# Kernel optimization log

Measured on AMD Instinct MI355X. Metric: run time of the kernel, lower is better.

## Reference

```python
import jax, jax.numpy as jnp
import numpy as np

B, S, HID, NH = 4, 2048, 2048, 16
HD = HID // NH
DECAY_INIT = 0.95


def setup_inputs() -> dict:
    key = jax.random.key(0)
    k1, k2, k3 = jax.random.split(key, 3)
    x = jax.random.normal(k1, (B, S, HID), jnp.float32)
    # torch Linear weights stored as [in, out] for x @ W; scaled like default init
    W_qkv = jax.random.normal(k2, (HID, 3 * HID), jnp.float32) / np.float32(np.sqrt(HID))
    W_out = jax.random.normal(k3, (HID, HID), jnp.float32) / np.float32(np.sqrt(HID))
    decay_param = jnp.full((NH,), DECAY_INIT, jnp.float32)
    kv0 = jnp.zeros((B, NH, HD), jnp.float32)
    k_sum0 = jnp.zeros((B, NH, HD), jnp.float32)
    attention_mask = jnp.ones((B, 1, 1, S), jnp.float32)
    return dict(x=x, kv0=kv0, k_sum0=k_sum0, attention_mask=attention_mask,
                W_qkv=W_qkv, W_out=W_out, decay_param=decay_param)


def _phi(u):
    # kernel feature map: elu(x) + 1 (non-negative)
    return jax.nn.elu(u) + 1.0


def reference(x, kv0, k_sum0, attention_mask, W_qkv, W_out, decay_param):
    b, s, hid = x.shape
    nh = decay_param.shape[0]
    hd = hid // nh
    qkv = x @ W_qkv                               # [b, s, 3*hid]
    q, k, v = jnp.split(qkv, 3, axis=-1)

    def to_time_major(t):                         # [b, s, hid] -> [s, b, nh, hd]
        return t.reshape(b, s, nh, hd).transpose(1, 0, 2, 3)

    q = _phi(to_time_major(q))
    k = _phi(to_time_major(k))
    v = to_time_major(v)

    # mask [b,1,1,s] -> [s, b, 1, 1]; padded tokens don't update the state
    m = attention_mask.reshape(b, 1, s, 1).transpose(2, 0, 1, 3)
    k = k * m
    v = v * m

    decay = jax.nn.sigmoid(decay_param)[None, :, None]  # [1, nh, 1]

    def step(carry, inp):
        kv, ks = carry                             # each [b, nh, hd]
        q_t, k_t, v_t = inp                        # each [b, nh, hd]
        kv = decay * kv + k_t * v_t
        ks = decay * ks + k_t
        num = jnp.sum(q_t * kv, axis=-1, keepdims=True)
        den = jnp.maximum(jnp.sum(q_t * ks, axis=-1, keepdims=True), 1e-6)
        return (kv, ks), (num / den) * q_t

    (kv, ks), outs = jax.lax.scan(step, (kv0, k_sum0), (q, k, v))
    out = outs.transpose(1, 0, 2, 3).reshape(b, s, hid) @ W_out
    return out, kv, ks
```

## Files before the change

kernel.cpp:

```cpp
#include <hip/hip_runtime.h>
#include <hip/hip_bf16.h>

typedef __hip_bfloat16 bf16;
typedef short bf16x8 __attribute__((ext_vector_type(8)));
typedef float f32x4 __attribute__((ext_vector_type(4)));

#define BB   4
#define SS   2048
#define HID  2048
#define NHD  16
#define HD   128
#define NCH  64
#define CHL  32

__device__ inline float sigm(float x) { return 1.f / (1.f + __expf(-x)); }
__device__ inline float phi_f(float v) { return v > 0.f ? v + 1.f : __expf(v); }

__device__ inline int probe_fp32(const void* probe) {
    return ((const unsigned*)probe)[0] != 0x3F733F73u;
}
__device__ inline float ldd(const void* p, int fp32, size_t i) {
    return fp32 ? ((const float*)p)[i] : __bfloat162float(((const bf16*)p)[i]);
}
__device__ inline void st_dual(void* p, int fp32, size_t i, float v) {
    if (fp32) ((float*)p)[i] = v;
    else      ((bf16*)p)[i] = __float2bfloat16(v);
}

__device__ inline void ld2(const bf16* p, float& a, float& b) {
    unsigned u = *(const unsigned*)p;
    union U { unsigned x; float f; } lo, hi;
    lo.x = u << 16; hi.x = u & 0xffff0000u;
    a = lo.f; b = hi.f;
}
__device__ inline void st2(bf16* p, float a, float b) {
    __hip_bfloat162 v;
    v.x = __float2bfloat16(a);
    v.y = __float2bfloat16(b);
    *(__hip_bfloat162*)p = v;
}

__device__ __forceinline__ void gload_lds16(const bf16* g, bf16* l) {
    __builtin_amdgcn_global_load_lds((const __attribute__((address_space(1))) void*)g,
                                     (__attribute__((address_space(3))) void*)l,
                                     16, 0, 0);
}

#define NB_CVT 16384
#define NB_T1  3072
#define NB_T2  1024
__global__ __launch_bounds__(256) void prep(const void* __restrict__ x,
                                            bf16* __restrict__ x_bf,
                                            const void* __restrict__ Wqkv,
                                            bf16* __restrict__ WqkvT,
                                            const void* __restrict__ Wout,
                                            bf16* __restrict__ WoutT,
                                            const void* __restrict__ probe) {
    int fp32 = probe_fp32(probe);
    int bid = blockIdx.x;
    int tid = threadIdx.x;
    if (bid < NB_CVT) {
        size_t i = ((size_t)bid * 256 + tid) * 4;
        if (fp32) {
            float4 v = *(const float4*)((const float*)x + i);
            bf16* o = x_bf + i;
            o[0] = __float2bfloat16(v.x); o[1] = __float2bfloat16(v.y);
            o[2] = __float2bfloat16(v.z); o[3] = __float2bfloat16(v.w);
        } else {
            *(short4*)(x_bf + i) = *(const short4*)((const bf16*)x + i);
        }
        return;
    }
    const void* in; bf16* out; int R, C, idx;
    if (bid < NB_CVT + NB_T1) {
        in = Wqkv; out = WqkvT; R = HID; C = 3 * HID; idx = bid - NB_CVT;
    } else {
        in = Wout; out = WoutT; R = HID; C = HID; idx = bid - NB_CVT - NB_T1;
    }
    int ctiles = C / 64;
    int c0 = (idx % ctiles) * 64;
    int r0 = (idx / ctiles) * 64;
    __shared__ bf16 t[64][65];
    int c = tid & 63;
    int rb = tid >> 6;
#pragma unroll
    for (int i = 0; i < 16; i++) {
        int r = rb + i * 4;
        t[r][c] = __float2bfloat16(ldd(in, fp32, (size_t)(r0 + r) * C + c0 + c));
    }
    __syncthreads();
#pragma unroll
    for (int i = 0; i < 16; i++) {
        int r = rb + i * 4;
        out[(size_t)(c0 + r) * R + r0 + c] = t[c][r];
    }
}

template <int MH>
__device__ __forceinline__ void lda_frags(const short* ldsA, bf16x8 (&af)[4][2],
                                          int wm2, int l15, int quad, int sw) {
#pragma unroll
    for (int i = 0; i < 4; i++) {
#pragma unroll
        for (int s = 0; s < 2; s++)
            af[i][s] = *(const bf16x8*)&ldsA[(MH * 128 + wm2 + i * 16 + l15) * 64 +
                                             (((quad + 4 * s) ^ sw) << 3)];
    }
}
template <int NH>
__device__ __forceinline__ void ldb_frags(const short* ldsB, bf16x8 (&bfr)[2][2],
                                          int wn2, int l15, int quad, int sw) {
#pragma unroll
    for (int j = 0; j < 2; j++) {
#pragma unroll
        for (int s = 0; s < 2; s++)
            bfr[j][s] = *(const bf16x8*)&ldsB[(NH * 128 + wn2 + j * 16 + l15) * 64 +
                                              (((quad + 4 * s) ^ sw) << 3)];
    }
}
template <int MH, int NH>
__device__ __forceinline__ void mma_quad(f32x4 (&acc)[2][2][4][2],
                                         const bf16x8 (&af)[4][2],
                                         const bf16x8 (&bfr)[2][2]) {
    __builtin_amdgcn_s_setprio(1);
#pragma unroll
    for (int s = 0; s < 2; s++)
#pragma unroll
        for (int i = 0; i < 4; i++)
#pragma unroll
            for (int j = 0; j < 2; j++)
                acc[MH][NH][i][j] = __builtin_amdgcn_mfma_f32_16x16x32_bf16(
                    af[i][s], bfr[j][s], acc[MH][NH][i][j], 0, 0, 0);
    __builtin_amdgcn_s_setprio(0);
}

template <int EPI>
__global__ __launch_bounds__(512) void gemm256(const bf16* __restrict__ A,
                                               const bf16* __restrict__ Bt,
                                               void* __restrict__ Cv,
                                               const void* __restrict__ mask,
                                               const void* __restrict__ probe,
                                               int M, int N, int K) {
    int fp32 = probe_fp32(probe);
    __shared__ __align__(16) short lds[2][2][256 * 64];
    const int tid = threadIdx.x;
    const int lane = tid & 63, wave = tid >> 6;
    const int quad = lane >> 4, l15 = lane & 15;
    const int sw = l15 & 7;
    const int wm2 = ((wave >> 2) & 1) * 64;
    const int wn2 = (wave & 3) * 32;
    const int m0 = blockIdx.y * 256, n0 = blockIdx.x * 256;
    const int KT = K >> 6;

    const int rl = lane >> 3, pu = lane & 7;
    const bf16* gAb = A  + (size_t)(m0 + wave * 8 + rl) * K + ((pu ^ rl) << 3);
    const bf16* gBb = Bt + (size_t)(n0 + wave * 8 + rl) * K + ((pu ^ rl) << 3);

    auto stageA = [&](int bufi, int h, int kt) {
        if (kt >= KT) return;
        const bf16* g = gAb + (size_t)(h * 128) * K + kt * 64;
        gload_lds16(g,                  (bf16*)&lds[bufi][0][(h * 128 + wave * 8) * 64]);
        gload_lds16(g + (size_t)64 * K, (bf16*)&lds[bufi][0][(h * 128 + 64 + wave * 8) * 64]);
    };
    auto stageB = [&](int bufi, int h, int kt) {
        if (kt >= KT) return;
        const bf16* g = gBb + (size_t)(h * 128) * K + kt * 64;
        gload_lds16(g,                  (bf16*)&lds[bufi][1][(h * 128 + wave * 8) * 64]);
        gload_lds16(g + (size_t)64 * K, (bf16*)&lds[bufi][1][(h * 128 + 64 + wave * 8) * 64]);
    };

    f32x4 acc[2][2][4][2];
    f32x4 zero = {0.f, 0.f, 0.f, 0.f};
#pragma unroll
    for (int a = 0; a < 2; a++)
#pragma unroll
        for (int b = 0; b < 2; b++)
#pragma unroll
            for (int i = 0; i < 4; i++)
#pragma unroll
                for (int j = 0; j < 2; j++) acc[a][b][i][j] = zero;
    bf16x8 af[4][2], bfr[2][2];

    stageA(0, 0, 0); stageB(0, 1, 0); stageA(0, 1, 0); stageB(0, 0, 0);
    stageA(1, 0, 1); stageB(1, 1, 1);
    asm volatile("s_waitcnt vmcnt(4)" ::: "memory");
    __builtin_amdgcn_s_barrier();

#define PH_SYNC_MFMA(MH, NH)                                                   \
    __builtin_amdgcn_sched_barrier(0);                                         \
    __builtin_amdgcn_s_barrier();                                              \
    asm volatile("s_waitcnt lgkmcnt(0)" ::: "memory");                         \
    __builtin_amdgcn_sched_barrier(0);                                         \
    mma_quad<MH, NH>(acc, af, bfr);                                            \
    __builtin_amdgcn_s_barrier();

#define TILE_BODY(BUF, kt)                                                     \
    {                                                                          \
        const short* ldsA = &lds[BUF][0][0];                                   \
        const short* ldsB = &lds[BUF][1][0];                                   \
                    \
        lda_frags<0>(ldsA, af, wm2, l15, quad, sw);                            \
        ldb_frags<0>(ldsB, bfr, wn2, l15, quad, sw);                           \
        stageA((BUF) ^ 1, 1, (kt) + 1);                                        \
        asm volatile("s_waitcnt lgkmcnt(8)" ::: "memory");                     \
        PH_SYNC_MFMA(0, 0)                                                     \
                            \
        ldb_frags<1>(ldsB, bfr, wn2, l15, quad, sw);                           \
        stageB((BUF) ^ 1, 0, (kt) + 1);                                        \
        PH_SYNC_MFMA(0, 1)                                                     \
           \
        lda_frags<1>(ldsA, af, wm2, l15, quad, sw);                            \
        stageA((BUF), 0, (kt) + 2);                                            \
        PH_SYNC_MFMA(1, 1)                                                     \
                         \
        ldb_frags<0>(ldsB, bfr, wn2, l15, quad, sw);                           \
        stageB((BUF), 1, (kt) + 2);                                            \
        __builtin_amdgcn_sched_barrier(0);                                     \
        __builtin_amdgcn_s_barrier();                                          \
        asm volatile("s_waitcnt lgkmcnt(0)" ::: "memory");                     \
        __builtin_amdgcn_sched_barrier(0);                                     \
        mma_quad<1, 0>(acc, af, bfr);                                          \
             \
        if ((kt) + 2 < KT) { asm volatile("s_waitcnt vmcnt(4)" ::: "memory"); }\
        else               { asm volatile("s_waitcnt vmcnt(0)" ::: "memory"); }\
        __builtin_amdgcn_s_barrier();                                          \
    }

    for (int kt = 0; kt < KT; kt += 2) {
        TILE_BODY(0, kt)
        TILE_BODY(1, kt + 1)
    }
#undef TILE_BODY
#undef PH_SYNC_MFMA

#pragma unroll
    for (int mh = 0; mh < 2; mh++)
#pragma unroll
        for (int i = 0; i < 4; i++)
#pragma unroll
            for (int r = 0; r < 4; r++) {
                int m = m0 + mh * 128 + wm2 + i * 16 + quad * 4 + r;
                float mk = 1.f;
                if (EPI) mk = ldd(mask, fp32, m);
#pragma unroll
                for (int nh = 0; nh < 2; nh++)
#pragma unroll
                    for (int j = 0; j < 2; j++) {
                        int n = n0 + nh * 128 + wn2 + j * 16 + l15;
                        float v = acc[mh][nh][i][j][r];
                        if (EPI) {
                            if (n < HID)          v = phi_f(v);
                            else if (n < 2 * HID) v = phi_f(v) * mk;
                            else                  v = v * mk;
                            ((bf16*)Cv)[(size_t)m * N + n] = __float2bfloat16(v);
                        } else {
                            st_dual(Cv, fp32, (size_t)m * N + n, v);
                        }
                    }
            }
}

__global__ __launch_bounds__(64) void scan_local(const bf16* __restrict__ qkv,
                                                 float* __restrict__ ckv,
                                                 float* __restrict__ cks,
                                                 const void* __restrict__ decp) {
    int fp32 = probe_fp32(decp);
    int blk = blockIdx.x;
    int bh = blk / NCH, c = blk % NCH;
    int b = bh >> 4, h = bh & 15;
    int lane = threadIdx.x;
    int hd = lane * 2;
    float dec = sigm(ldd(decp, fp32, h));
    const bf16* kb = qkv + (size_t)(b * SS + c * CHL) * (3 * HID) + HID + h * HD + hd;
    const bf16* vb = kb + HID;
    float kv0 = 0.f, kv1 = 0.f, ks0 = 0.f, ks1 = 0.f;
    for (int t = 0; t < CHL; t++) {
        float k0, k1, v0, v1;
        ld2(kb, k0, k1);
        ld2(vb, v0, v1);
        kb += 3 * HID; vb += 3 * HID;
        kv0 = dec * kv0 + k0 * v0;
        kv1 = dec * kv1 + k1 * v1;
        ks0 = dec * ks0 + k0;
        ks1 = dec * ks1 + k1;
    }
    int o = blk * HD + hd;
    ckv[o] = kv0; ckv[o + 1] = kv1;
    cks[o] = ks0; cks[o + 1] = ks1;
}

__global__ __launch_bounds__(64) void scan_out(const bf16* __restrict__ qkv,
                                               const float* __restrict__ ckv,
                                               const float* __restrict__ cks,
                                               const void* __restrict__ kv0in,
                                               const void* __restrict__ ks0in,
                                               const void* __restrict__ decp,
                                               bf16* __restrict__ outs,
                                               void* __restrict__ outbase) {
    int fp32 = probe_fp32(decp);
    int blk = blockIdx.x;
    int bh = blk / NCH, c = blk % NCH;
    int b = bh >> 4, h = bh & 15;
    int lane = threadIdx.x;
    int hd = lane * 2;
    float dec = sigm(ldd(decp, fp32, h));
    float dl = powf(dec, (float)CHL);

    float kva = ldd(kv0in, fp32, bh * HD + hd);
    float kvb = ldd(kv0in, fp32, bh * HD + hd + 1);
    float ksa = ldd(ks0in, fp32, bh * HD + hd);
    float ksb = ldd(ks0in, fp32, bh * HD + hd + 1);
    for (int j = 0; j < c; j++) {
        int o = (bh * NCH + j) * HD + hd;
        kva = dl * kva + ckv[o];
        kvb = dl * kvb + ckv[o + 1];
        ksa = dl * ksa + cks[o];
        ksb = dl * ksb + cks[o + 1];
    }

    const bf16* qb = qkv + (size_t)(b * SS + c * CHL) * (3 * HID) + h * HD + hd;
    const bf16* kb = qb + HID;
    const bf16* vb = qb + 2 * HID;
    bf16* ob = outs + (size_t)(b * SS + c * CHL) * HID + h * HD + hd;
    for (int t = 0; t < CHL; t++) {
        float q0, q1, k0, k1, v0, v1;
        ld2(qb, q0, q1);
        ld2(kb, k0, k1);
        ld2(vb, v0, v1);
        qb += 3 * HID; kb += 3 * HID; vb += 3 * HID;
        kva = dec * kva + k0 * v0;
        kvb = dec * kvb + k1 * v1;
        ksa = dec * ksa + k0;
        ksb = dec * ksb + k1;
        float num = q0 * kva + q1 * kvb;
        float den = q0 * ksa + q1 * ksb;
#pragma unroll
        for (int off = 32; off > 0; off >>= 1) {
            num += __shfl_xor(num, off);
            den += __shfl_xor(den, off);
        }
        float sc = num / fmaxf(den, 1e-6f);
        st2(ob, q0 * sc, q1 * sc);
        ob += HID;
    }

    if (c == NCH - 1) {
        size_t base = (size_t)BB * SS * HID;
        st_dual(outbase, fp32, base + bh * HD + hd, kva);
        st_dual(outbase, fp32, base + bh * HD + hd + 1, kvb);
        st_dual(outbase, fp32, base + BB * NHD * HD + bh * HD + hd, ksa);
        st_dual(outbase, fp32, base + BB * NHD * HD + bh * HD + hd + 1, ksb);
    }
}

extern "C" void kernel_launch(void* const* d_in, const int* in_sizes, int n_in,
                              void* d_out, int out_size, void* d_ws, size_t ws_size,
                              hipStream_t stream) {
    const void* x    = d_in[0];
    const void* kv0  = d_in[1];
    const void* ks0  = d_in[2];
    const void* am   = d_in[3];
    const void* Wqkv = d_in[4];
    const void* Wout = d_in[5];
    const void* decp = d_in[6];

    const int M = BB * SS;
    const int N1 = 3 * HID;
    const int K = HID;

    char* ws = (char*)d_ws;
    bf16* WqkvT = (bf16*)ws;  ws += (size_t)N1 * K * 2;
    bf16* WoutT = (bf16*)ws;  ws += (size_t)HID * HID * 2;
    bf16* x_bf  = (bf16*)ws;  ws += (size_t)M * HID * 2;
    bf16* qkvb  = (bf16*)ws;  ws += (size_t)M * N1 * 2;
    bf16* outs  = (bf16*)ws;  ws += (size_t)M * HID * 2;
    float* ckv  = (float*)ws; ws += (size_t)BB * NHD * NCH * HD * 4;
    float* cks  = (float*)ws; ws += (size_t)BB * NHD * NCH * HD * 4;

    prep<<<NB_CVT + NB_T1 + NB_T2, 256, 0, stream>>>(x, x_bf, Wqkv, WqkvT,
                                                     Wout, WoutT, decp);

    gemm256<1><<<dim3(N1 / 256, M / 256), 512, 0, stream>>>(x_bf, WqkvT, qkvb, am, decp,
                                                            M, N1, K);

    scan_local<<<BB * NHD * NCH, 64, 0, stream>>>(qkvb, ckv, cks, decp);
    scan_out<<<BB * NHD * NCH, 64, 0, stream>>>(qkvb, ckv, cks, kv0, ks0, decp,
                                                outs, d_out);

    gemm256<0><<<dim3(HID / 256, M / 256), 512, 0, stream>>>(outs, WoutT, d_out, nullptr,
                                                             decp, M, HID, K);
}
```

Before: 505.1 us.

## Halve scan chunk length and pack two chunks per wavefront with 4-wide loads

The chunked linear-attention scan now uses 128 chunks of 16 steps instead of 64 chunks of 32, which halves the serial per-chunk recurrence. Each 64-lane wavefront now handles two (batch,head,chunk) items, with each lane covering 4 head dims through 8-byte bf16 loads and stores and float4 chunk-state accesses. The shuffle reduction shrinks to 5 steps. The cost is a longer serial prefix over preceding chunk states in scan_out (up to 127 iterations) and twice as many chunk-state reads.

```diff
diff --git a/kernel.cpp b/kernel.cpp
--- a/kernel.cpp
+++ b/kernel.cpp
@@ -10,8 +10,8 @@
 #define HID  2048
 #define NHD  16
 #define HD   128
-#define NCH  64
-#define CHL  32
+#define NCH  128
+#define CHL  16
 
 __device__ inline float sigm(float x) { return 1.f / (1.f + __expf(-x)); }
 __device__ inline float phi_f(float v) { return v > 0.f ? v + 1.f : __expf(v); }
@@ -27,17 +27,21 @@
     else      ((bf16*)p)[i] = __float2bfloat16(v);
 }
 
-__device__ inline void ld2(const bf16* p, float& a, float& b) {
-    unsigned u = *(const unsigned*)p;
-    union U { unsigned x; float f; } lo, hi;
-    lo.x = u << 16; hi.x = u & 0xffff0000u;
-    a = lo.f; b = hi.f;
-}
-__device__ inline void st2(bf16* p, float a, float b) {
-    __hip_bfloat162 v;
-    v.x = __float2bfloat16(a);
-    v.y = __float2bfloat16(b);
-    *(__hip_bfloat162*)p = v;
+__device__ inline void ld4b(const bf16* p, float& a, float& b, float& c, float& d) {
+    uint2 u = *(const uint2*)p;
+    union U { unsigned x; float f; } t;
+    t.x = u.x << 16;          a = t.f;
+    t.x = u.x & 0xffff0000u;  b = t.f;
+    t.x = u.y << 16;          c = t.f;
+    t.x = u.y & 0xffff0000u;  d = t.f;
+}
+__device__ inline void st4b(bf16* p, float a, float b, float c, float d) {
+    __hip_bfloat162 lo, hi;
+    lo.x = __float2bfloat16(a); lo.y = __float2bfloat16(b);
+    hi.x = __float2bfloat16(c); hi.y = __float2bfloat16(d);
+    uint2 u;
+    u.x = *(unsigned*)&lo; u.y = *(unsigned*)&hi;
+    *(uint2*)p = u;
 }
 
 __device__ __forceinline__ void gload_lds16(const bf16* g, bf16* l) {
@@ -265,28 +269,30 @@
                                                  float* __restrict__ cks,
                                                  const void* __restrict__ decp) {
     int fp32 = probe_fp32(decp);
-    int blk = blockIdx.x;
-    int bh = blk / NCH, c = blk % NCH;
+    int lane = threadIdx.x;
+    int p = blockIdx.x * 2 + (lane >> 5);
+    int c = p >> 6;
+    int bh = p & 63;
     int b = bh >> 4, h = bh & 15;
-    int lane = threadIdx.x;
-    int hd = lane * 2;
+    int hd = (lane & 31) * 4;
     float dec = sigm(ldd(decp, fp32, h));
     const bf16* kb = qkv + (size_t)(b * SS + c * CHL) * (3 * HID) + HID + h * HD + hd;
     const bf16* vb = kb + HID;
-    float kv0 = 0.f, kv1 = 0.f, ks0 = 0.f, ks1 = 0.f;
+    float kv0 = 0.f, kv1 = 0.f, kv2 = 0.f, kv3 = 0.f;
+    float ks0 = 0.f, ks1 = 0.f, ks2 = 0.f, ks3 = 0.f;
     for (int t = 0; t < CHL; t++) {
-        float k0, k1, v0, v1;
-        ld2(kb, k0, k1);
-        ld2(vb, v0, v1);
+        float k0, k1, k2, k3, v0, v1, v2, v3;
+        ld4b(kb, k0, k1, k2, k3);
+        ld4b(vb, v0, v1, v2, v3);
         kb += 3 * HID; vb += 3 * HID;
-        kv0 = dec * kv0 + k0 * v0;
-        kv1 = dec * kv1 + k1 * v1;
-        ks0 = dec * ks0 + k0;
-        ks1 = dec * ks1 + k1;
-    }
-    int o = blk * HD + hd;
-    ckv[o] = kv0; ckv[o + 1] = kv1;
-    cks[o] = ks0; cks[o + 1] = ks1;
+        kv0 = dec * kv0 + k0 * v0;  kv1 = dec * kv1 + k1 * v1;
+        kv2 = dec * kv2 + k2 * v2;  kv3 = dec * kv3 + k3 * v3;
+        ks0 = dec * ks0 + k0;       ks1 = dec * ks1 + k1;
+        ks2 = dec * ks2 + k2;       ks3 = dec * ks3 + k3;
+    }
+    size_t o = (size_t)(bh * NCH + c) * HD + hd;
+    *(float4*)&ckv[o] = make_float4(kv0, kv1, kv2, kv3);
+    *(float4*)&cks[o] = make_float4(ks0, ks1, ks2, ks3);
 }
 
 __global__ __launch_bounds__(64) void scan_out(const bf16* __restrict__ qkv,
@@ -298,24 +304,31 @@
                                                bf16* __restrict__ outs,
                                                void* __restrict__ outbase) {
     int fp32 = probe_fp32(decp);
-    int blk = blockIdx.x;
-    int bh = blk / NCH, c = blk % NCH;
+    int lane = threadIdx.x;
+    int p = blockIdx.x * 2 + (lane >> 5);
+    int c = p >> 6;
+    int bh = p & 63;
     int b = bh >> 4, h = bh & 15;
-    int lane = threadIdx.x;
-    int hd = lane * 2;
+    int hd = (lane & 31) * 4;
     float dec = sigm(ldd(decp, fp32, h));
     float dl = powf(dec, (float)CHL);
 
     float kva = ldd(kv0in, fp32, bh * HD + hd);
     float kvb = ldd(kv0in, fp32, bh * HD + hd + 1);
+    float kvc = ldd(kv0in, fp32, bh * HD + hd + 2);
+    float kvd = ldd(kv0in, fp32, bh * HD + hd + 3);
     float ksa = ldd(ks0in, fp32, bh * HD + hd);
     float ksb = ldd(ks0in, fp32, bh * HD + hd + 1);
+    float ksc = ldd(ks0in, fp32, bh * HD + hd + 2);
+    float ksd = ldd(ks0in, fp32, bh * HD + hd + 3);
     for (int j = 0; j < c; j++) {
-        int o = (bh * NCH + j) * HD + hd;
-        kva = dl * kva + ckv[o];
-        kvb = dl * kvb + ckv[o + 1];
-        ksa = dl * ksa + cks[o];
-        ksb = dl * ksb + cks[o + 1];
+        size_t o = (size_t)(bh * NCH + j) * HD + hd;
+        float4 fv = *(const float4*)&ckv[o];
+        float4 fs = *(const float4*)&cks[o];
+        kva = dl * kva + fv.x;  kvb = dl * kvb + fv.y;
+        kvc = dl * kvc + fv.z;  kvd = dl * kvd + fv.w;
+        ksa = dl * ksa + fs.x;  ksb = dl * ksb + fs.y;
+        ksc = dl * ksc + fs.z;  ksd = dl * ksd + fs.w;
     }
 
     const bf16* qb = qkv + (size_t)(b * SS + c * CHL) * (3 * HID) + h * HD + hd;
@@ -323,33 +336,37 @@
     const bf16* vb = qb + 2 * HID;
     bf16* ob = outs + (size_t)(b * SS + c * CHL) * HID + h * HD + hd;
     for (int t = 0; t < CHL; t++) {
-        float q0, q1, k0, k1, v0, v1;
-        ld2(qb, q0, q1);
-        ld2(kb, k0, k1);
-        ld2(vb, v0, v1);
+        float q0, q1, q2, q3, k0, k1, k2, k3, v0, v1, v2, v3;
+        ld4b(qb, q0, q1, q2, q3);
+        ld4b(kb, k0, k1, k2, k3);
+        ld4b(vb, v0, v1, v2, v3);
         qb += 3 * HID; kb += 3 * HID; vb += 3 * HID;
-        kva = dec * kva + k0 * v0;
-        kvb = dec * kvb + k1 * v1;
-        ksa = dec * ksa + k0;
-        ksb = dec * ksb + k1;
-        float num = q0 * kva + q1 * kvb;
-        float den = q0 * ksa + q1 * ksb;
-#pragma unroll
-        for (int off = 32; off > 0; off >>= 1) {
+        kva = dec * kva + k0 * v0;  kvb = dec * kvb + k1 * v1;
+        kvc = dec * kvc + k2 * v2;  kvd = dec * kvd + k3 * v3;
+        ksa = dec * ksa + k0;       ksb = dec * ksb + k1;
+        ksc = dec * ksc + k2;       ksd = dec * ksd + k3;
+        float num = q0 * kva + q1 * kvb + q2 * kvc + q3 * kvd;
+        float den = q0 * ksa + q1 * ksb + q2 * ksc + q3 * ksd;
+#pragma unroll
+        for (int off = 16; off > 0; off >>= 1) {
             num += __shfl_xor(num, off);
             den += __shfl_xor(den, off);
         }
         float sc = num / fmaxf(den, 1e-6f);
-        st2(ob, q0 * sc, q1 * sc);
+        st4b(ob, q0 * sc, q1 * sc, q2 * sc, q3 * sc);
         ob += HID;
     }
 
     if (c == NCH - 1) {
         size_t base = (size_t)BB * SS * HID;
-        st_dual(outbase, fp32, base + bh * HD + hd, kva);
+        st_dual(outbase, fp32, base + bh * HD + hd,     kva);
         st_dual(outbase, fp32, base + bh * HD + hd + 1, kvb);
-        st_dual(outbase, fp32, base + BB * NHD * HD + bh * HD + hd, ksa);
+        st_dual(outbase, fp32, base + bh * HD + hd + 2, kvc);
+        st_dual(outbase, fp32, base + bh * HD + hd + 3, kvd);
+        st_dual(outbase, fp32, base + BB * NHD * HD + bh * HD + hd,     ksa);
         st_dual(outbase, fp32, base + BB * NHD * HD + bh * HD + hd + 1, ksb);
+        st_dual(outbase, fp32, base + BB * NHD * HD + bh * HD + hd + 2, ksc);
+        st_dual(outbase, fp32, base + BB * NHD * HD + bh * HD + hd + 3, ksd);
     }
 }
 
@@ -383,9 +400,9 @@
     gemm256<1><<<dim3(N1 / 256, M / 256), 512, 0, stream>>>(x_bf, WqkvT, qkvb, am, decp,
                                                             M, N1, K);
 
-    scan_local<<<BB * NHD * NCH, 64, 0, stream>>>(qkvb, ckv, cks, decp);
-    scan_out<<<BB * NHD * NCH, 64, 0, stream>>>(qkvb, ckv, cks, kv0, ks0, decp,
-                                                outs, d_out);
+    scan_local<<<BB * NHD * NCH / 2, 64, 0, stream>>>(qkvb, ckv, cks, decp);
+    scan_out<<<BB * NHD * NCH / 2, 64, 0, stream>>>(qkvb, ckv, cks, kv0, ks0, decp,
+                                                    outs, d_out);
 
     gemm256<0><<<dim3(HID / 256, M / 256), 512, 0, stream>>>(outs, WoutT, d_out, nullptr,
                                                              decp, M, HID, K);
```

After: 508.9 us. Within noise of the previous version (+0.8%).
